# Kernel optimization log

Hardware: AMD Instinct MI355X
Metric: run time of the kernel (lower is better)

## Reference

```python
import jax, jax.numpy as jnp
import numpy as np

N, D, K_FRAC = 4096, 256, 0.5
EPS = 1e-5  # BatchNorm1d default eps


def setup_inputs() -> dict:
    key = jax.random.key(0)
    kg, kh, kw = jax.random.split(key, 3)
    # sparse binary adjacency with self-loops so all degrees > 0 (pow(D,-1) finite)
    g = (jax.random.uniform(kg, (N, N)) < 0.004).astype(jnp.float32)
    g = jnp.maximum(g, jnp.eye(N, dtype=jnp.float32))
    h = jax.random.normal(kh, (N, D), dtype=jnp.float32)
    return {
        "g": g,
        "h": h,
        "gamma": jnp.ones((D,), jnp.float32),
        "beta": jnp.zeros((D,), jnp.float32),
        "w_proj": jax.random.normal(kw, (D, 1), dtype=jnp.float32) / np.sqrt(D),
        "b_proj": jnp.zeros((1,), jnp.float32),
        "sigma1": jnp.array([0.2], jnp.float32),
    }


def reference(g, h, gamma, beta, w_proj, b_proj, sigma1):
    # BatchNorm1d in training mode: batch statistics over the node axis
    mu = h.mean(0)
    var = h.var(0)  # biased variance, as torch uses for normalization
    h = (h - mu) / jnp.sqrt(var + EPS) * gamma + beta

    deg = g.sum(1)                               # [N] == Z2
    agg = (g @ h) / deg[:, None]                 # diag(D^-1) @ (g @ h), no NxN diag materialized
    Z1 = jnp.abs(h - agg).sum(1)                 # [N]
    pl = jax.nn.sigmoid(Z1 + deg)
    Z3 = (agg @ w_proj + b_proj)[:, 0]           # proj(Z3).squeeze()
    pg = jax.nn.softmax(Z3)                      # 1-D softmax (dim 0)
    pt = jax.nn.sigmoid(pl + pg)
    pf = jax.nn.sigmoid((h @ w_proj + b_proj)[:, 0])
    scores = sigma1[0] * pt + (1.0 - sigma1[0]) * pf

    # top_k_graph
    k = max(2, int(K_FRAC * N))
    _, idx = jax.lax.top_k(scores, k)            # [k]
    h_att = scores[:, None] * h                  # score-weighted features
    un_g = (g != 0).astype(jnp.float32)
    two_hop = ((un_g @ un_g) != 0).astype(jnp.float32)  # binarized 2-hop adjacency
    a_hat = two_hop[idx, :]                      # [k, N] row gather
    new_h = a_hat @ h_att                        # [k, D]
    g_new = a_hat[:, idx]                        # [k, k] column gather
    # norm_g: torch broadcast divides COLUMN j by row-sum degrees[j]
    g_new = g_new / g_new.sum(1)
    return g_new, new_h, idx
```

## Files before the change

kernel.cpp:

```cpp
#include <hip/hip_runtime.h>
#include <math.h>

#define NN 4096
#define DD 256
#define KK 2048
#define NW 64

__device__ __forceinline__ int build_list(const unsigned long long* __restrict__ B, int r,
                                          int l, int* cols, int cap) {
    unsigned long long word = B[(size_t)r * NW + l];
    int pc = __popcll(word);
    int off = pc;
    for (int d = 1; d < 64; d <<= 1) {
        int n = __shfl_up(off, d);
        if (l >= d) off += n;
    }
    int total = __shfl(off, 63);
    int base = off - pc;
    while (word) {
        int b = (int)__ffsll(word) - 1;
        word &= word - 1;
        if (base < cap) cols[base] = l * 64 + b;
        ++base;
    }
    return total;
}

__global__ void k_pre(const float* __restrict__ h, const float* __restrict__ g,
                      double* __restrict__ psum, double* __restrict__ psq,
                      unsigned long long* __restrict__ B) {
    int blk = blockIdx.x;
    int t = threadIdx.x;
    if (blk < 64) {
        int d = t;
        int r0 = blk * 64;
        double s0=0,s1=0,s2=0,s3=0,q0=0,q1=0,q2=0,q3=0;
        for (int k = 0; k < 64; k += 4) {
            double x0 = (double)h[(size_t)(r0+k+0) * DD + d];
            double x1 = (double)h[(size_t)(r0+k+1) * DD + d];
            double x2 = (double)h[(size_t)(r0+k+2) * DD + d];
            double x3 = (double)h[(size_t)(r0+k+3) * DD + d];
            s0 += x0; q0 += x0*x0;
            s1 += x1; q1 += x1*x1;
            s2 += x2; q2 += x2*x2;
            s3 += x3; q3 += x3*x3;
        }
        psum[blk * DD + d] = (s0+s1)+(s2+s3);
        psq [blk * DD + d] = (q0+q1)+(q2+q3);
    } else {
        int i = blk - 64;
        int q = t >> 6, l = t & 63;
        const float4* g4 = (const float4*)(g + (size_t)i * NN);
        for (int wi = 0; wi < 4; ++wi) {
            float4 v = g4[q * 256 + wi * 64 + l];
            unsigned int nib = (unsigned int)(v.x != 0.f)
                             | ((unsigned int)(v.y != 0.f) << 1)
                             | ((unsigned int)(v.z != 0.f) << 2)
                             | ((unsigned int)(v.w != 0.f) << 3);
            unsigned long long word = (unsigned long long)nib << (4 * (l & 15));
            unsigned int lo = (unsigned int)word, hi = (unsigned int)(word >> 32);
            for (int s = 1; s < 16; s <<= 1) {
                lo |= __shfl_xor(lo, s, 16);
                hi |= __shfl_xor(hi, s, 16);
            }
            if ((l & 15) == 0)
                B[(size_t)i * NW + 16 * q + 4 * wi + (l >> 4)] =
                    ((unsigned long long)hi << 32) | lo;
        }
    }
}

__global__ void k_stats_final(const double* __restrict__ psum, const double* __restrict__ psq,
                              double* __restrict__ mu, double* __restrict__ rstd) {
    __shared__ double rs[4][DD];
    __shared__ double rq[4][DD];
    int t = threadIdx.x;
    int d = t & (DD - 1);
    int q = t >> 8;
    double s0=0,s1=0,q0=0,q1=0;
    int b0 = q * 16;
    for (int k = 0; k < 16; k += 2) {
        s0 += psum[(b0+k)   * DD + d];
        s1 += psum[(b0+k+1) * DD + d];
        q0 += psq [(b0+k)   * DD + d];
        q1 += psq [(b0+k+1) * DD + d];
    }
    rs[q][d] = s0 + s1;
    rq[q][d] = q0 + q1;
    __syncthreads();
    if (q == 0) {
        double S  = (rs[0][d]+rs[1][d]) + (rs[2][d]+rs[3][d]);
        double Q  = (rq[0][d]+rq[1][d]) + (rq[2][d]+rq[3][d]);
        double m  = S / (double)NN;
        double var = Q / (double)NN - m * m;
        mu[d]   = m;
        rstd[d] = 1.0 / sqrt(var + 1e-5);
    }
}

__global__ void k_main(const float* __restrict__ h, const double* __restrict__ mu,
                       const double* __restrict__ rstd, const float* __restrict__ gamma,
                       const float* __restrict__ beta, const unsigned long long* __restrict__ Bm,
                       const float* __restrict__ w, const float* __restrict__ bp,
                       float* __restrict__ hn, double* __restrict__ zpf,
                       unsigned long long* __restrict__ T, double* __restrict__ Z1,
                       double* __restrict__ Z3, int* __restrict__ degi) {
    __shared__ int cols[4][136];
    int blk = blockIdx.x;
    int t = threadIdx.x;
    int wv = t >> 6, l = t & 63;
    if (blk < 1024) {
        int r = blk * 4 + wv;
        int cnt = build_list(Bm, r, l, cols[wv], 128);
        if (cnt > 128) cnt = 128;
        const float4* h4 = (const float4*)h;
        double s0=0,s1=0,s2=0,s3=0;
        double u0=0,u1=0,u2=0,u3=0;
        int j = 0;
        for (; j + 3 < cnt; j += 4) {
            float4 v0 = h4[(size_t)cols[wv][j]     * 64 + l];
            float4 v1 = h4[(size_t)cols[wv][j + 1] * 64 + l];
            float4 v2 = h4[(size_t)cols[wv][j + 2] * 64 + l];
            float4 v3 = h4[(size_t)cols[wv][j + 3] * 64 + l];
            s0 += (double)v0.x; s1 += (double)v0.y; s2 += (double)v0.z; s3 += (double)v0.w;
            u0 += (double)v1.x; u1 += (double)v1.y; u2 += (double)v1.z; u3 += (double)v1.w;
            s0 += (double)v2.x; s1 += (double)v2.y; s2 += (double)v2.z; s3 += (double)v2.w;
            u0 += (double)v3.x; u1 += (double)v3.y; u2 += (double)v3.z; u3 += (double)v3.w;
        }
        for (; j < cnt; ++j) {
            float4 v0 = h4[(size_t)cols[wv][j] * 64 + l];
            s0 += (double)v0.x; s1 += (double)v0.y; s2 += (double)v0.z; s3 += (double)v0.w;
        }
        s0 += u0; s1 += u1; s2 += u2; s3 += u3;
        const double2* mu2 = (const double2*)mu;
        const double2* rs2 = (const double2*)rstd;
        const float4*  ga4 = (const float4*)gamma;
        const float4*  be4 = (const float4*)beta;
        const float4*  w4  = (const float4*)w;
        double2 mA = mu2[2*l], mB = mu2[2*l+1];
        double2 rA = rs2[2*l], rB = rs2[2*l+1];
        float4 ga = ga4[l], be = be4[l], wl = w4[l];
        double inv = 1.0 / (double)cnt;
        double g0 = (s0 * inv - mA.x) * rA.x * (double)ga.x + (double)be.x;
        double g1 = (s1 * inv - mA.y) * rA.y * (double)ga.y + (double)be.y;
        double g2 = (s2 * inv - mB.x) * rB.x * (double)ga.z + (double)be.z;
        double g3 = (s3 * inv - mB.y) * rB.y * (double)ga.w + (double)be.w;
        float4 hv = h4[(size_t)r * 64 + l];
        double h0 = ((double)hv.x - mA.x) * rA.x * (double)ga.x + (double)be.x;
        double h1 = ((double)hv.y - mA.y) * rA.y * (double)ga.y + (double)be.y;
        double h2 = ((double)hv.z - mB.x) * rB.x * (double)ga.z + (double)be.z;
        double h3 = ((double)hv.w - mB.y) * rB.y * (double)ga.w + (double)be.w;
        float4 o = { (float)h0, (float)h1, (float)h2, (float)h3 };
        ((float4*)hn)[(size_t)r * 64 + l] = o;
        double z1p = (fabs(h0 - g0) + fabs(h1 - g1)) + (fabs(h2 - g2) + fabs(h3 - g3));
        double z3p = (g0 * (double)wl.x + g1 * (double)wl.y)
                   + (g2 * (double)wl.z + g3 * (double)wl.w);
        double zfp = (h0 * (double)wl.x + h1 * (double)wl.y)
                   + (h2 * (double)wl.z + h3 * (double)wl.w);
        for (int off = 32; off > 0; off >>= 1) {
            z1p += __shfl_down(z1p, off);
            z3p += __shfl_down(z3p, off);
            zfp += __shfl_down(zfp, off);
        }
        if (l == 0) {
            Z1[r] = z1p;
            Z3[r] = z3p + (double)bp[0];
            zpf[r] = zfp + (double)bp[0];
            degi[r] = cnt;
        }
    } else {
        int r = (blk - 1024) * 4 + wv;
        int cnt = build_list(Bm, r, l, cols[wv], 128);
        if (cnt > 128) cnt = 128;
        unsigned long long a0 = 0ull, a1 = 0ull, a2 = 0ull, a3 = 0ull;
        int j = 0;
        for (; j + 3 < cnt; j += 4) {
            a0 |= Bm[(size_t)cols[wv][j]     * NW + l];
            a1 |= Bm[(size_t)cols[wv][j + 1] * NW + l];
            a2 |= Bm[(size_t)cols[wv][j + 2] * NW + l];
            a3 |= Bm[(size_t)cols[wv][j + 3] * NW + l];
        }
        for (; j < cnt; ++j) a0 |= Bm[(size_t)cols[wv][j] * NW + l];
        T[(size_t)r * NW + l] = (a0 | a1) | (a2 | a3);
    }
}

__global__ void k_scorekeys(const double* __restrict__ Z1, const double* __restrict__ Z3,
                            const double* __restrict__ zpf, const int* __restrict__ degi,
                            const float* __restrict__ sigma1, float* __restrict__ scores,
                            unsigned long long* __restrict__ keys) {
    __shared__ double red[256];
    int t = threadIdx.x;
    double mx = -1e300;
    for (int k = 0; k < 16; ++k) mx = fmax(mx, Z3[t + 256 * k]);
    red[t] = mx;
    __syncthreads();
    for (int s = 128; s > 0; s >>= 1) {
        if (t < s) red[t] = fmax(red[t], red[t + s]);
        __syncthreads();
    }
    double M = red[0];
    __syncthreads();
    double se = 0.0;
    for (int k = 0; k < 16; ++k) se += exp(Z3[t + 256 * k] - M);
    red[t] = se;
    __syncthreads();
    for (int s = 128; s > 0; s >>= 1) {
        if (t < s) red[t] += red[t + s];
        __syncthreads();
    }
    double sum = red[0];
    int i = blockIdx.x * 256 + t;
    double s1 = (double)sigma1[0];
    double pg = exp(Z3[i] - M) / sum;
    double pl = 1.0 / (1.0 + exp(-(Z1[i] + (double)degi[i])));
    double pt = 1.0 / (1.0 + exp(-(pl + pg)));
    double pf = 1.0 / (1.0 + exp(-zpf[i]));
    float sc = (float)(s1 * pt + (1.0 - s1) * pf);
    scores[i] = sc;
    unsigned int b2 = __float_as_uint(sc);
    unsigned int ka = (b2 & 0x80000000u) ? ~b2 : (b2 ^ 0x80000000u);
    keys[i] = ((unsigned long long)(~ka) << 32) | (unsigned int)i;
}

__global__ void k_rank(const unsigned long long* __restrict__ keys, int* __restrict__ idx_int,
                       float* __restrict__ out_idx) {
    __shared__ unsigned long long Kl[NN];
    int t = threadIdx.x;
    for (int i = t; i < NN; i += 256) Kl[i] = keys[i];
    __syncthreads();
    int il = t >> 4, sub = t & 15;
    int i = blockIdx.x * 16 + il;
    unsigned long long ki = Kl[i];
    int c0 = 0, c1 = 0, c2 = 0, c3 = 0;
    for (int jj = 0; jj < 256; jj += 4) {
        int j = sub + (jj << 4);
        c0 += (Kl[j]      < ki) ? 1 : 0;
        c1 += (Kl[j + 16] < ki) ? 1 : 0;
        c2 += (Kl[j + 32] < ki) ? 1 : 0;
        c3 += (Kl[j + 48] < ki) ? 1 : 0;
    }
    int cnt = (c0 + c1) + (c2 + c3);
    for (int off = 8; off > 0; off >>= 1) cnt += __shfl_down(cnt, off, 16);
    if (sub == 0 && cnt < KK) {
        idx_int[cnt] = i;
        out_idx[cnt] = (float)i;
    }
}

__global__ void k_rowsum(const unsigned long long* __restrict__ T, const int* __restrict__ idx_int,
                         float* __restrict__ inv_rs) {
    __shared__ unsigned long long Sl[NW];
    int t = threadIdx.x;
    Sl[t] = 0ull;
    for (int j = t; j < KK; j += 64) {
        int ii = idx_int[j];
        atomicOr(&Sl[ii >> 6], 1ull << (ii & 63));
    }
    int j = blockIdx.x * 64 + t;
    int r = idx_int[j];
    const unsigned long long* Tr = T + (size_t)r * NW;
    int c0 = 0, c1 = 0, c2 = 0, c3 = 0;
    for (int w = 0; w < NW; w += 4) {
        c0 += __popcll(Tr[w]     & Sl[w]);
        c1 += __popcll(Tr[w + 1] & Sl[w + 1]);
        c2 += __popcll(Tr[w + 2] & Sl[w + 2]);
        c3 += __popcll(Tr[w + 3] & Sl[w + 3]);
    }
    inv_rs[j] = 1.0f / (float)((c0 + c1) + (c2 + c3));
}

__global__ void k_out(const unsigned long long* __restrict__ T, const int* __restrict__ idx_int,
                      const float* __restrict__ inv_rs, const float* __restrict__ scores,
                      const float* __restrict__ hn, float* __restrict__ out_gnew,
                      float* __restrict__ out_newh) {
    __shared__ unsigned long long Tl[NW];
    __shared__ int cols[2048];
    __shared__ int s_cnt;
    __shared__ float4 red[4][64];
    int blk = blockIdx.x;
    int t = threadIdx.x;
    if (blk < KK) {
        int r = blk;
        if (t < NW) Tl[t] = T[(size_t)idx_int[r] * NW + t];
        __syncthreads();
        const int4*   idx4 = (const int4*)idx_int;
        const float4* irs4 = (const float4*)inv_rs;
        float4* out4 = (float4*)(out_gnew + (size_t)r * KK);
        for (int c4 = t; c4 < KK / 4; c4 += 256) {
            int4 jc = idx4[c4];
            float4 iv = irs4[c4];
            float4 o;
            o.x = ((Tl[jc.x >> 6] >> (jc.x & 63)) & 1ull) ? iv.x : 0.0f;
            o.y = ((Tl[jc.y >> 6] >> (jc.y & 63)) & 1ull) ? iv.y : 0.0f;
            o.z = ((Tl[jc.z >> 6] >> (jc.z & 63)) & 1ull) ? iv.z : 0.0f;
            o.w = ((Tl[jc.w >> 6] >> (jc.w & 63)) & 1ull) ? iv.w : 0.0f;
            out4[c4] = o;
        }
    } else {
        int r = blk - KK;
        int wv = t >> 6, l = t & 63;
        if (t < 64) {
            int total = build_list(T, idx_int[r], t, cols, 2048);
            if (t == 63) s_cnt = total;
        }
        __syncthreads();
        int cnt = s_cnt < 2048 ? s_cnt : 2048;
        const float4* hn4 = (const float4*)hn;
        float4 a0 = {0,0,0,0}, a1 = {0,0,0,0}, a2 = {0,0,0,0}, a3 = {0,0,0,0};
        float4 a4 = {0,0,0,0}, a5 = {0,0,0,0}, a6 = {0,0,0,0}, a7 = {0,0,0,0};
        int j = wv;
        for (; j + 28 < cnt; j += 32) {
            int c0 = cols[j],      c1 = cols[j + 4],  c2 = cols[j + 8],  c3 = cols[j + 12];
            int c4 = cols[j + 16], c5 = cols[j + 20], c6 = cols[j + 24], c7 = cols[j + 28];
            float s0 = scores[c0], s1 = scores[c1], s2 = scores[c2], s3 = scores[c3];
            float s4 = scores[c4], s5 = scores[c5], s6 = scores[c6], s7 = scores[c7];
            float4 v0 = hn4[(size_t)c0 * 64 + l];
            float4 v1 = hn4[(size_t)c1 * 64 + l];
            float4 v2 = hn4[(size_t)c2 * 64 + l];
            float4 v3 = hn4[(size_t)c3 * 64 + l];
            float4 v4 = hn4[(size_t)c4 * 64 + l];
            float4 v5 = hn4[(size_t)c5 * 64 + l];
            float4 v6 = hn4[(size_t)c6 * 64 + l];
            float4 v7 = hn4[(size_t)c7 * 64 + l];
            a0.x = fmaf(s0, v0.x, a0.x); a0.y = fmaf(s0, v0.y, a0.y);
            a0.z = fmaf(s0, v0.z, a0.z); a0.w = fmaf(s0, v0.w, a0.w);
            a1.x = fmaf(s1, v1.x, a1.x); a1.y = fmaf(s1, v1.y, a1.y);
            a1.z = fmaf(s1, v1.z, a1.z); a1.w = fmaf(s1, v1.w, a1.w);
            a2.x = fmaf(s2, v2.x, a2.x); a2.y = fmaf(s2, v2.y, a2.y);
            a2.z = fmaf(s2, v2.z, a2.z); a2.w = fmaf(s2, v2.w, a2.w);
            a3.x = fmaf(s3, v3.x, a3.x); a3.y = fmaf(s3, v3.y, a3.y);
            a3.z = fmaf(s3, v3.z, a3.z); a3.w = fmaf(s3, v3.w, a3.w);
            a4.x = fmaf(s4, v4.x, a4.x); a4.y = fmaf(s4, v4.y, a4.y);
            a4.z = fmaf(s4, v4.z, a4.z); a4.w = fmaf(s4, v4.w, a4.w);
            a5.x = fmaf(s5, v5.x, a5.x); a5.y = fmaf(s5, v5.y, a5.y);
            a5.z = fmaf(s5, v5.z, a5.z); a5.w = fmaf(s5, v5.w, a5.w);
            a6.x = fmaf(s6, v6.x, a6.x); a6.y = fmaf(s6, v6.y, a6.y);
            a6.z = fmaf(s6, v6.z, a6.z); a6.w = fmaf(s6, v6.w, a6.w);
            a7.x = fmaf(s7, v7.x, a7.x); a7.y = fmaf(s7, v7.y, a7.y);
            a7.z = fmaf(s7, v7.z, a7.z); a7.w = fmaf(s7, v7.w, a7.w);
        }
        for (; j < cnt; j += 4) {
            int c0 = cols[j];
            float s0 = scores[c0];
            float4 v0 = hn4[(size_t)c0 * 64 + l];
            a0.x = fmaf(s0, v0.x, a0.x); a0.y = fmaf(s0, v0.y, a0.y);
            a0.z = fmaf(s0, v0.z, a0.z); a0.w = fmaf(s0, v0.w, a0.w);
        }
        float4 acc;
        acc.x = ((a0.x + a1.x) + (a2.x + a3.x)) + ((a4.x + a5.x) + (a6.x + a7.x));
        acc.y = ((a0.y + a1.y) + (a2.y + a3.y)) + ((a4.y + a5.y) + (a6.y + a7.y));
        acc.z = ((a0.z + a1.z) + (a2.z + a3.z)) + ((a4.z + a5.z) + (a6.z + a7.z));
        acc.w = ((a0.w + a1.w) + (a2.w + a3.w)) + ((a4.w + a5.w) + (a6.w + a7.w));
        red[wv][l] = acc;
        __syncthreads();
        if (t < 64) {
            float4 r0 = red[0][t], r1 = red[1][t], r2 = red[2][t], r3 = red[3][t];
            float4 o;
            o.x = (r0.x + r1.x) + (r2.x + r3.x);
            o.y = (r0.y + r1.y) + (r2.y + r3.y);
            o.z = (r0.z + r1.z) + (r2.z + r3.z);
            o.w = (r0.w + r1.w) + (r2.w + r3.w);
            ((float4*)(out_newh + (size_t)r * DD))[t] = o;
        }
    }
}

extern "C" void kernel_launch(void* const* d_in, const int* in_sizes, int n_in,
                              void* d_out, int out_size, void* d_ws, size_t ws_size,
                              hipStream_t stream) {
    const float* g      = (const float*)d_in[0];
    const float* h      = (const float*)d_in[1];
    const float* gamma  = (const float*)d_in[2];
    const float* beta   = (const float*)d_in[3];
    const float* w_proj = (const float*)d_in[4];
    const float* b_proj = (const float*)d_in[5];
    const float* sigma1 = (const float*)d_in[6];

    char* p = (char*)d_ws;
    auto alloc = [&](size_t bytes) -> void* {
        void* q = (void*)p;
        p += (bytes + 255) & ~(size_t)255;
        return q;
    };
    double* mu      = (double*)alloc(DD * 8);
    double* rstd    = (double*)alloc(DD * 8);
    double* psum    = (double*)alloc(64 * DD * 8);
    double* psq     = (double*)alloc(64 * DD * 8);
    double* zpf     = (double*)alloc(NN * 8);
    double* Z1      = (double*)alloc(NN * 8);
    double* Z3      = (double*)alloc(NN * 8);
    int*    degi    = (int*)alloc(NN * 4);
    float*  scores  = (float*)alloc(NN * 4);
    unsigned long long* keys = (unsigned long long*)alloc(NN * 8);
    int*    idx_int = (int*)alloc(KK * 4);
    float*  inv_rs  = (float*)alloc(KK * 4);
    unsigned long long* B = (unsigned long long*)alloc((size_t)NN * NW * 8);
    unsigned long long* T = (unsigned long long*)alloc((size_t)NN * NW * 8);
    float*  hn      = (float*)alloc((size_t)NN * DD * 4);

    float* out_gnew = (float*)d_out;
    float* out_newh = out_gnew + (size_t)KK * KK;
    float* out_idx  = out_newh + (size_t)KK * DD;

    hipLaunchKernelGGL(k_pre,         dim3(64 + NN), dim3(256),  0, stream, h, g, psum, psq, B);
    hipLaunchKernelGGL(k_stats_final, dim3(1),       dim3(1024), 0, stream, psum, psq, mu, rstd);
    hipLaunchKernelGGL(k_main,        dim3(2048),    dim3(256),  0, stream, h, mu, rstd, gamma, beta, B, w_proj, b_proj, hn, zpf, T, Z1, Z3, degi);
    hipLaunchKernelGGL(k_scorekeys,   dim3(16),      dim3(256),  0, stream, Z1, Z3, zpf, degi, sigma1, scores, keys);
    hipLaunchKernelGGL(k_rank,        dim3(256),     dim3(256),  0, stream, keys, idx_int, out_idx);
    hipLaunchKernelGGL(k_rowsum,      dim3(32),      dim3(64),   0, stream, T, idx_int, inv_rs);
    hipLaunchKernelGGL(k_out,         dim3(2 * KK),  dim3(256),  0, stream, T, idx_int, inv_rs, scores, hn, out_gnew, out_newh);
}
```

Measured before the change: 181.1 us.

## Fuse score computation into rank kernel and repartition new_h gather per wave

```diff
diff --git a/kernel.cpp b/kernel.cpp
--- a/kernel.cpp
+++ b/kernel.cpp
@@ -185,12 +185,14 @@
     }
 }
 
-__global__ void k_scorekeys(const double* __restrict__ Z1, const double* __restrict__ Z3,
+__global__ void k_scorerank(const double* __restrict__ Z1, const double* __restrict__ Z3,
                             const double* __restrict__ zpf, const int* __restrict__ degi,
                             const float* __restrict__ sigma1, float* __restrict__ scores,
-                            unsigned long long* __restrict__ keys) {
+                            int* __restrict__ idx_int, float* __restrict__ out_idx) {
     __shared__ double red[256];
-    int t = threadIdx.x;
+    __shared__ unsigned long long Kl[NN];
+    int t = threadIdx.x;
+    int blk = blockIdx.x;
     double mx = -1e300;
     for (int k = 0; k < 16; ++k) mx = fmax(mx, Z3[t + 256 * k]);
     red[t] = mx;
@@ -210,27 +212,22 @@
         __syncthreads();
     }
     double sum = red[0];
-    int i = blockIdx.x * 256 + t;
     double s1 = (double)sigma1[0];
-    double pg = exp(Z3[i] - M) / sum;
-    double pl = 1.0 / (1.0 + exp(-(Z1[i] + (double)degi[i])));
-    double pt = 1.0 / (1.0 + exp(-(pl + pg)));
-    double pf = 1.0 / (1.0 + exp(-zpf[i]));
-    float sc = (float)(s1 * pt + (1.0 - s1) * pf);
-    scores[i] = sc;
-    unsigned int b2 = __float_as_uint(sc);
-    unsigned int ka = (b2 & 0x80000000u) ? ~b2 : (b2 ^ 0x80000000u);
-    keys[i] = ((unsigned long long)(~ka) << 32) | (unsigned int)i;
-}
-
-__global__ void k_rank(const unsigned long long* __restrict__ keys, int* __restrict__ idx_int,
-                       float* __restrict__ out_idx) {
-    __shared__ unsigned long long Kl[NN];
-    int t = threadIdx.x;
-    for (int i = t; i < NN; i += 256) Kl[i] = keys[i];
+    for (int k = 0; k < 16; ++k) {
+        int i = t + 256 * k;
+        double pg = exp(Z3[i] - M) / sum;
+        double pl = 1.0 / (1.0 + exp(-(Z1[i] + (double)degi[i])));
+        double pt = 1.0 / (1.0 + exp(-(pl + pg)));
+        double pf = 1.0 / (1.0 + exp(-zpf[i]));
+        float sc = (float)(s1 * pt + (1.0 - s1) * pf);
+        if ((i >> 4) == blk) scores[i] = sc;
+        unsigned int b2 = __float_as_uint(sc);
+        unsigned int ka = (b2 & 0x80000000u) ? ~b2 : (b2 ^ 0x80000000u);
+        Kl[i] = ((unsigned long long)(~ka) << 32) | (unsigned int)i;
+    }
     __syncthreads();
     int il = t >> 4, sub = t & 15;
-    int i = blockIdx.x * 16 + il;
+    int i = blk * 16 + il;
     unsigned long long ki = Kl[i];
     int c0 = 0, c1 = 0, c2 = 0, c3 = 0;
     for (int jj = 0; jj < 256; jj += 4) {
@@ -275,9 +272,7 @@
                       const float* __restrict__ hn, float* __restrict__ out_gnew,
                       float* __restrict__ out_newh) {
     __shared__ unsigned long long Tl[NW];
-    __shared__ int cols[2048];
-    __shared__ int s_cnt;
-    __shared__ float4 red[4][64];
+    __shared__ int cols4[4][2048];
     int blk = blockIdx.x;
     int t = threadIdx.x;
     if (blk < KK) {
@@ -298,71 +293,44 @@
             out4[c4] = o;
         }
     } else {
-        int r = blk - KK;
+        int b  = blk - KK;
+        int dt = b & 3;
+        int rg = b >> 2;
         int wv = t >> 6, l = t & 63;
-        if (t < 64) {
-            int total = build_list(T, idx_int[r], t, cols, 2048);
-            if (t == 63) s_cnt = total;
-        }
-        __syncthreads();
-        int cnt = s_cnt < 2048 ? s_cnt : 2048;
+        int r  = rg * 4 + wv;
+        int* cols = cols4[wv];
+        int cnt = build_list(T, idx_int[r], l, cols, 2048);
+        if (cnt > 2048) cnt = 2048;
+        int sub = l & 15;
+        int grp = l >> 4;
         const float4* hn4 = (const float4*)hn;
-        float4 a0 = {0,0,0,0}, a1 = {0,0,0,0}, a2 = {0,0,0,0}, a3 = {0,0,0,0};
-        float4 a4 = {0,0,0,0}, a5 = {0,0,0,0}, a6 = {0,0,0,0}, a7 = {0,0,0,0};
-        int j = wv;
-        for (; j + 28 < cnt; j += 32) {
-            int c0 = cols[j],      c1 = cols[j + 4],  c2 = cols[j + 8],  c3 = cols[j + 12];
-            int c4 = cols[j + 16], c5 = cols[j + 20], c6 = cols[j + 24], c7 = cols[j + 28];
-            float s0 = scores[c0], s1 = scores[c1], s2 = scores[c2], s3 = scores[c3];
-            float s4 = scores[c4], s5 = scores[c5], s6 = scores[c6], s7 = scores[c7];
-            float4 v0 = hn4[(size_t)c0 * 64 + l];
-            float4 v1 = hn4[(size_t)c1 * 64 + l];
-            float4 v2 = hn4[(size_t)c2 * 64 + l];
-            float4 v3 = hn4[(size_t)c3 * 64 + l];
-            float4 v4 = hn4[(size_t)c4 * 64 + l];
-            float4 v5 = hn4[(size_t)c5 * 64 + l];
-            float4 v6 = hn4[(size_t)c6 * 64 + l];
-            float4 v7 = hn4[(size_t)c7 * 64 + l];
+        int dbase = dt * 16;
+        float4 a0 = {0,0,0,0}, a1 = {0,0,0,0};
+        int j = grp;
+        for (; j + 4 < cnt; j += 8) {
+            int c0 = cols[j], c1 = cols[j + 4];
+            float s0 = scores[c0], s1 = scores[c1];
+            float4 v0 = hn4[(size_t)c0 * 64 + dbase + sub];
+            float4 v1 = hn4[(size_t)c1 * 64 + dbase + sub];
             a0.x = fmaf(s0, v0.x, a0.x); a0.y = fmaf(s0, v0.y, a0.y);
             a0.z = fmaf(s0, v0.z, a0.z); a0.w = fmaf(s0, v0.w, a0.w);
             a1.x = fmaf(s1, v1.x, a1.x); a1.y = fmaf(s1, v1.y, a1.y);
             a1.z = fmaf(s1, v1.z, a1.z); a1.w = fmaf(s1, v1.w, a1.w);
-            a2.x = fmaf(s2, v2.x, a2.x); a2.y = fmaf(s2, v2.y, a2.y);
-            a2.z = fmaf(s2, v2.z, a2.z); a2.w = fmaf(s2, v2.w, a2.w);
-            a3.x = fmaf(s3, v3.x, a3.x); a3.y = fmaf(s3, v3.y, a3.y);
-            a3.z = fmaf(s3, v3.z, a3.z); a3.w = fmaf(s3, v3.w, a3.w);
-            a4.x = fmaf(s4, v4.x, a4.x); a4.y = fmaf(s4, v4.y, a4.y);
-            a4.z = fmaf(s4, v4.z, a4.z); a4.w = fmaf(s4, v4.w, a4.w);
-            a5.x = fmaf(s5, v5.x, a5.x); a5.y = fmaf(s5, v5.y, a5.y);
-            a5.z = fmaf(s5, v5.z, a5.z); a5.w = fmaf(s5, v5.w, a5.w);
-            a6.x = fmaf(s6, v6.x, a6.x); a6.y = fmaf(s6, v6.y, a6.y);
-            a6.z = fmaf(s6, v6.z, a6.z); a6.w = fmaf(s6, v6.w, a6.w);
-            a7.x = fmaf(s7, v7.x, a7.x); a7.y = fmaf(s7, v7.y, a7.y);
-            a7.z = fmaf(s7, v7.z, a7.z); a7.w = fmaf(s7, v7.w, a7.w);
         }
         for (; j < cnt; j += 4) {
             int c0 = cols[j];
             float s0 = scores[c0];
-            float4 v0 = hn4[(size_t)c0 * 64 + l];
+            float4 v0 = hn4[(size_t)c0 * 64 + dbase + sub];
             a0.x = fmaf(s0, v0.x, a0.x); a0.y = fmaf(s0, v0.y, a0.y);
             a0.z = fmaf(s0, v0.z, a0.z); a0.w = fmaf(s0, v0.w, a0.w);
         }
-        float4 acc;
-        acc.x = ((a0.x + a1.x) + (a2.x + a3.x)) + ((a4.x + a5.x) + (a6.x + a7.x));
-        acc.y = ((a0.y + a1.y) + (a2.y + a3.y)) + ((a4.y + a5.y) + (a6.y + a7.y));
-        acc.z = ((a0.z + a1.z) + (a2.z + a3.z)) + ((a4.z + a5.z) + (a6.z + a7.z));
-        acc.w = ((a0.w + a1.w) + (a2.w + a3.w)) + ((a4.w + a5.w) + (a6.w + a7.w));
-        red[wv][l] = acc;
-        __syncthreads();
-        if (t < 64) {
-            float4 r0 = red[0][t], r1 = red[1][t], r2 = red[2][t], r3 = red[3][t];
-            float4 o;
-            o.x = (r0.x + r1.x) + (r2.x + r3.x);
-            o.y = (r0.y + r1.y) + (r2.y + r3.y);
-            o.z = (r0.z + r1.z) + (r2.z + r3.z);
-            o.w = (r0.w + r1.w) + (r2.w + r3.w);
-            ((float4*)(out_newh + (size_t)r * DD))[t] = o;
-        }
+        a0.x += a1.x; a0.y += a1.y; a0.z += a1.z; a0.w += a1.w;
+        a0.x += __shfl_xor(a0.x, 16); a0.y += __shfl_xor(a0.y, 16);
+        a0.z += __shfl_xor(a0.z, 16); a0.w += __shfl_xor(a0.w, 16);
+        a0.x += __shfl_xor(a0.x, 32); a0.y += __shfl_xor(a0.y, 32);
+        a0.z += __shfl_xor(a0.z, 32); a0.w += __shfl_xor(a0.w, 32);
+        if (grp == 0)
+            ((float4*)(out_newh + (size_t)r * DD))[dbase + sub] = a0;
     }
 }
 
@@ -392,7 +360,6 @@
     double* Z3      = (double*)alloc(NN * 8);
     int*    degi    = (int*)alloc(NN * 4);
     float*  scores  = (float*)alloc(NN * 4);
-    unsigned long long* keys = (unsigned long long*)alloc(NN * 8);
     int*    idx_int = (int*)alloc(KK * 4);
     float*  inv_rs  = (float*)alloc(KK * 4);
     unsigned long long* B = (unsigned long long*)alloc((size_t)NN * NW * 8);
@@ -406,8 +373,7 @@
     hipLaunchKernelGGL(k_pre,         dim3(64 + NN), dim3(256),  0, stream, h, g, psum, psq, B);
     hipLaunchKernelGGL(k_stats_final, dim3(1),       dim3(1024), 0, stream, psum, psq, mu, rstd);
     hipLaunchKernelGGL(k_main,        dim3(2048),    dim3(256),  0, stream, h, mu, rstd, gamma, beta, B, w_proj, b_proj, hn, zpf, T, Z1, Z3, degi);
-    hipLaunchKernelGGL(k_scorekeys,   dim3(16),      dim3(256),  0, stream, Z1, Z3, zpf, degi, sigma1, scores, keys);
-    hipLaunchKernelGGL(k_rank,        dim3(256),     dim3(256),  0, stream, keys, idx_int, out_idx);
+    hipLaunchKernelGGL(k_scorerank,   dim3(256),     dim3(256),  0, stream, Z1, Z3, zpf, degi, sigma1, scores, idx_int, out_idx);
     hipLaunchKernelGGL(k_rowsum,      dim3(32),      dim3(64),   0, stream, T, idx_int, inv_rs);
     hipLaunchKernelGGL(k_out,         dim3(2 * KK),  dim3(256),  0, stream, T, idx_int, inv_rs, scores, hn, out_gnew, out_newh);
 }
```

Result: slower. 190.2 us (+5.0%).
